# Kernel tuning notes

Measured on AMD Instinct MI355X. Metric: run time of the kernel, lower is better.

## Reference

```python
import jax, jax.numpy as jnp
from jax import lax
import numpy as np

DIM, RESO, HEADS, SPLIT, B = 128, 112, 4, 7, 2
HID = 4 * DIM  # mlp_ratio=4


def _ln(x, g, b):
    m = x.mean(-1, keepdims=True)
    v = ((x - m) ** 2).mean(-1, keepdims=True)
    return (x - m) * lax.rsqrt(v + 1e-5) * g + b


def _lepe_attn(q, k, v, cw, cb, H, W, H_sp, W_sp, nh):
    # q,k,v: [B, H*W, C] (C = branch dim); cw: depthwise conv weight [C,1,3,3]
    Bq, L, C = q.shape
    hd = C // nh
    scale = hd ** -0.5
    nHw, nWw = H // H_sp, W // W_sp

    def to_win(t):  # [B,H,W,C] -> [B*nHw*nWw, nh, H_sp*W_sp, hd]
        t = t.reshape(Bq, nHw, H_sp, nWw, W_sp, C).transpose(0, 1, 3, 2, 4, 5)
        return t.reshape(-1, H_sp * W_sp, nh, hd).transpose(0, 2, 1, 3)

    qw = to_win(q.reshape(Bq, H, W, C)) * scale
    kw = to_win(k.reshape(Bq, H, W, C))

    # v path: window partition in NCHW, depthwise conv LePE per window
    vimg = v.transpose(0, 2, 1).reshape(Bq, C, H, W)
    vimg = vimg.reshape(Bq, C, nHw, H_sp, nWw, W_sp).transpose(0, 2, 4, 1, 3, 5)
    vimg = vimg.reshape(-1, C, H_sp, W_sp)  # [B', C, H_sp, W_sp]
    lepe = lax.conv_general_dilated(vimg, cw, (1, 1), 'SAME', feature_group_count=C,
                                    dimension_numbers=('NCHW', 'OIHW', 'NCHW'))
    lepe = lepe + cb[None, :, None, None]
    vw = vimg.reshape(-1, nh, hd, H_sp * W_sp).transpose(0, 1, 3, 2)
    lepe = lepe.reshape(-1, nh, hd, H_sp * W_sp).transpose(0, 1, 3, 2)

    attn = jax.nn.softmax(jnp.einsum('whnd,whmd->whnm', qw, kw), axis=-1)
    o = jnp.einsum('whnm,whmd->whnd', attn, vw) + lepe  # [B', nh, S, hd]

    # windows2img
    o = o.transpose(0, 2, 1, 3).reshape(-1, H_sp * W_sp, C)
    o = o.reshape(Bq, nHw, nWw, H_sp, W_sp, C).transpose(0, 1, 3, 2, 4, 5)
    return o.reshape(Bq, H * W, C)


def setup_inputs() -> dict:
    key = jax.random.key(0)
    ks = jax.random.split(key, 16)
    s = 0.02
    Cb = DIM // 2
    return {
        'x': jax.random.normal(ks[0], (B, RESO * RESO, DIM), jnp.float32),
        'g1': jnp.ones((DIM,), jnp.float32),
        'b1': jnp.zeros((DIM,), jnp.float32),
        'w_qkv': s * jax.random.normal(ks[1], (3 * DIM, DIM), jnp.float32),
        'conv_w0': s * jax.random.normal(ks[2], (Cb, 1, 3, 3), jnp.float32),
        'conv_b0': jnp.zeros((Cb,), jnp.float32),
        'conv_w1': s * jax.random.normal(ks[3], (Cb, 1, 3, 3), jnp.float32),
        'conv_b1': jnp.zeros((Cb,), jnp.float32),
        'w_proj': s * jax.random.normal(ks[4], (DIM, DIM), jnp.float32),
        'b_proj': jnp.zeros((DIM,), jnp.float32),
        'g2': jnp.ones((DIM,), jnp.float32),
        'b2': jnp.zeros((DIM,), jnp.float32),
        'w_fc1': s * jax.random.normal(ks[5], (HID, DIM), jnp.float32),
        'b_fc1': jnp.zeros((HID,), jnp.float32),
        'w_fc2': s * jax.random.normal(ks[6], (DIM, HID), jnp.float32),
        'b_fc2': jnp.zeros((DIM,), jnp.float32),
    }


def reference(x, g1, b1, w_qkv, conv_w0, conv_b0, conv_w1, conv_b1,
              w_proj, b_proj, g2, b2, w_fc1, b_fc1, w_fc2, b_fc2):
    Bq, L, C = x.shape
    Cb = C // 2
    nh_b = HEADS // 2
    img = _ln(x, g1, b1)
    qkv = (img @ w_qkv.T).reshape(Bq, L, 3, C)  # qkv_bias=False
    q, k, v = qkv[:, :, 0], qkv[:, :, 1], qkv[:, :, 2]
    # branch 0: horizontal stripes (H_sp=RESO, W_sp=SPLIT) on first half of channels
    x1 = _lepe_attn(q[..., :Cb], k[..., :Cb], v[..., :Cb], conv_w0, conv_b0,
                    RESO, RESO, RESO, SPLIT, nh_b)
    # branch 1: vertical stripes (H_sp=SPLIT, W_sp=RESO) on second half
    x2 = _lepe_attn(q[..., Cb:], k[..., Cb:], v[..., Cb:], conv_w1, conv_b1,
                    RESO, RESO, SPLIT, RESO, nh_b)
    att = jnp.concatenate([x1, x2], axis=2)
    att = att @ w_proj.T + b_proj
    x = x + att  # drop_path = identity (prob 0)
    y = _ln(x, g2, b2)
    h = jax.nn.gelu(y @ w_fc1.T + b_fc1, approximate=False)
    x = x + (h @ w_fc2.T + b_fc2)
    return x
```

## Files before the change

### kernel.cpp

```cpp
#include <hip/hip_runtime.h>
#include <cstdint>

#define LTOK 12544
#define BATCH 2
#define CDIM 128
#define C3 384
#define RES 112
#define NROWS (BATCH * LTOK)
#define SCALE 0.17677669529663687f

typedef __attribute__((ext_vector_type(8))) short bf16x8;
typedef __attribute__((ext_vector_type(4))) float f32x4;

__device__ inline ushort f2b(float f) {
    union { float f; unsigned u; } v; v.f = f;
    unsigned r = (v.u + 0x7FFFu + ((v.u >> 16) & 1u)) >> 16;
    return (ushort)r;
}
__device__ inline float b2f(ushort u) {
    union { float f; unsigned u; } v; v.u = ((unsigned)u) << 16; return v.f;
}
__device__ inline float gelu_f(float a) {
    return 0.5f * a * (1.0f + erff(a * 0.70710678118654752f));
}

__device__ inline void nij(int n, int branch, int& i, int& j) {
    if (branch == 0) { i = n / 7; j = n - i * 7; }
    else             { i = n / 112; j = n - i * 112; }
}

__global__ __launch_bounds__(256) void k_cvt(const float* __restrict__ w0, const float* __restrict__ w1,
        const float* __restrict__ w2, const float* __restrict__ w3,
        ushort* __restrict__ o0, ushort* __restrict__ o1,
        ushort* __restrict__ o2, ushort* __restrict__ o3)
{
    int idx = blockIdx.x * 256 + threadIdx.x;
    const float* src; ushort* dst; int vi;
    if      (idx < 12288) { src = w0; dst = o0; vi = idx; }
    else if (idx < 16384) { src = w1; dst = o1; vi = idx - 12288; }
    else if (idx < 32768) { src = w2; dst = o2; vi = idx - 16384; }
    else                  { src = w3; dst = o3; vi = idx - 32768; }
    float4 v = ((const float4*)src)[vi];
    ushort4 r; r.x = f2b(v.x); r.y = f2b(v.y); r.z = f2b(v.z); r.w = f2b(v.w);
    ((ushort4*)dst)[vi] = r;
}

__global__ __launch_bounds__(256) void k_ln_qkv(const float* __restrict__ x,
        const float* __restrict__ g1, const float* __restrict__ b1,
        const ushort* __restrict__ wqkv_bf, ushort* __restrict__ qkv)
{
    __shared__ ushort ys[32][136];
    const int tid = threadIdx.x;
    const long long row0 = (long long)blockIdx.x * 32;

    {
        const int r = tid >> 3, l8 = tid & 7;
        const float* xr = x + (row0 + r) * CDIM + l8 * 16;
        float4 a[4];
        #pragma unroll
        for (int i = 0; i < 4; ++i) a[i] = ((const float4*)xr)[i];
        float s = 0.f, s2 = 0.f;
        #pragma unroll
        for (int i = 0; i < 4; ++i) {
            s  += a[i].x + a[i].y + a[i].z + a[i].w;
            s2 += a[i].x*a[i].x + a[i].y*a[i].y + a[i].z*a[i].z + a[i].w*a[i].w;
        }
        #pragma unroll
        for (int m = 4; m >= 1; m >>= 1) { s += __shfl_xor(s, m, 8); s2 += __shfl_xor(s2, m, 8); }
        const float mean = s * (1.f / 128.f);
        const float var = s2 * (1.f / 128.f) - mean * mean;
        const float rs = rsqrtf(var + 1e-5f);
        ushort4 w[4];
        #pragma unroll
        for (int i = 0; i < 4; ++i) {
            float4 gg = *(const float4*)(g1 + l8 * 16 + i * 4);
            float4 bb = *(const float4*)(b1 + l8 * 16 + i * 4);
            w[i].x = f2b((a[i].x - mean) * rs * gg.x + bb.x);
            w[i].y = f2b((a[i].y - mean) * rs * gg.y + bb.y);
            w[i].z = f2b((a[i].z - mean) * rs * gg.z + bb.z);
            w[i].w = f2b((a[i].w - mean) * rs * gg.w + bb.w);
        }
        #pragma unroll
        for (int i = 0; i < 4; ++i) *(ushort4*)&ys[r][l8 * 16 + i * 4] = w[i];
    }
    __syncthreads();

    const int wv = tid >> 6, lane = tid & 63;
    const int c16 = lane & 15, g = lane >> 4;

    bf16x8 yb[2][4];
    #pragma unroll
    for (int mt = 0; mt < 2; ++mt)
        #pragma unroll
        for (int kc = 0; kc < 4; ++kc)
            yb[mt][kc] = *(const bf16x8*)&ys[mt * 16 + c16][kc * 32 + g * 8];

    #pragma unroll
    for (int t = 0; t < 6; ++t) {
        const int n0 = wv * 96 + t * 16;
        bf16x8 aw[4];
        #pragma unroll
        for (int kc = 0; kc < 4; ++kc)
            aw[kc] = *(const bf16x8*)&wqkv_bf[(n0 + c16) * CDIM + kc * 32 + g * 8];
        #pragma unroll
        for (int mt = 0; mt < 2; ++mt) {
            f32x4 acc = {0.f, 0.f, 0.f, 0.f};
            #pragma unroll
            for (int kc = 0; kc < 4; ++kc)
                acc = __builtin_amdgcn_mfma_f32_16x16x32_bf16(aw[kc], yb[mt][kc], acc, 0, 0, 0);
            ushort4 sv;
            sv.x = f2b(acc[0]); sv.y = f2b(acc[1]); sv.z = f2b(acc[2]); sv.w = f2b(acc[3]);
            *(ushort4*)&qkv[(row0 + mt * 16 + c16) * C3 + n0 + g * 4] = sv;
        }
    }
}

__global__ __launch_bounds__(256) void k_attn_mfma(const ushort* __restrict__ qkv,
        const float* __restrict__ cw0, const float* __restrict__ cb0,
        const float* __restrict__ cw1, const float* __restrict__ cb1,
        ushort* __restrict__ att)
{
    __shared__ __align__(16) ushort ks[112 * 40];
    __shared__ __align__(16) ushort vt[32 * 136];
    __shared__ __align__(16) ushort pl[4][16 * 40];
    __shared__ __align__(16) float  ol[4][16 * 36];

    const int tid = threadIdx.x;
    const int wv = tid >> 6, lane = tid & 63;
    const int g = lane >> 4, c16 = lane & 15;

    const int wh = blockIdx.x;
    const int branch = wh >> 6;
    const int idx = wh & 63;
    const int win = idx >> 1, head = idx & 1;
    const int b = win >> 4, w = win & 15;
    const int rowBase = branch ? w * 7 : 0;
    const int colBase = branch ? 0 : w * 7;
    const float* cw = branch ? cw1 : cw0;
    const float* cb = branch ? cb1 : cb0;
    const int cbase = branch * 64 + head * 32;
    const long long qkvB = (long long)b * LTOK * C3;

    {
        const int row = tid >> 3, cwd = tid & 7;
        *(unsigned*)&vt[row * 136 + 112 + cwd * 2] = 0u;
    }

    const int t0 = blockIdx.y * 7 + 2 * wv;
    const int nt = (2 * wv + 1 < 7) ? 2 : 1;

    bf16x8 qf[2];
    #pragma unroll
    for (int t = 0; t < 2; ++t) if (t < nt) {
        int n = (t0 + t) * 16 + c16;
        int i, j; nij(n, branch, i, j);
        const ushort* qp = qkv + qkvB + (long long)((rowBase + i) * RES + colBase + j) * C3 + cbase + g * 8;
        bf16x8 qq = *(const bf16x8*)qp;
        #pragma unroll
        for (int e = 0; e < 8; ++e) qq[e] = (short)f2b(b2f((ushort)qq[e]) * SCALE);
        qf[t] = qq;
    }

    f32x4 O00 = {0.f,0.f,0.f,0.f}, O01 = {0.f,0.f,0.f,0.f};
    f32x4 O10 = {0.f,0.f,0.f,0.f}, O11 = {0.f,0.f,0.f,0.f};
    float lsum0[4] = {0.f,0.f,0.f,0.f};
    float lsum1[4] = {0.f,0.f,0.f,0.f};

    for (int cc = 0; cc < 7; ++cc) {
        __syncthreads();
        for (int u = tid; u < 448; u += 256) {
            const int key = u >> 2, d8 = (u & 3) * 8;
            const int n = cc * 112 + key;
            int i, j; nij(n, branch, i, j);
            const ushort* base = qkv + qkvB + (long long)((rowBase + i) * RES + colBase + j) * C3 + cbase + d8;
            bf16x8 kk = *(const bf16x8*)(base + 128);
            bf16x8 vv = *(const bf16x8*)(base + 256);
            *(bf16x8*)&ks[key * 40 + d8] = kk;
            #pragma unroll
            for (int e = 0; e < 8; ++e) vt[(d8 + e) * 136 + key] = (ushort)vv[e];
        }
        __syncthreads();

        #pragma unroll
        for (int p = 0; p < 4; ++p) {
            bf16x8 kf0 = *(const bf16x8*)&ks[(p * 32 + c16) * 40 + g * 8];
            bf16x8 kf1;
            if (p < 3) kf1 = *(const bf16x8*)&ks[(p * 32 + 16 + c16) * 40 + g * 8];
            bf16x8 vf0 = *(const bf16x8*)&vt[c16 * 136 + p * 32 + g * 8];
            bf16x8 vf1 = *(const bf16x8*)&vt[(16 + c16) * 136 + p * 32 + g * 8];
            ushort* pb = &pl[wv][0];

            #pragma unroll
            for (int t = 0; t < 2; ++t) if (t < nt) {
                const bf16x8 qq = t ? qf[1] : qf[0];
                f32x4 z = {0.f,0.f,0.f,0.f};
                f32x4 S0 = __builtin_amdgcn_mfma_f32_16x16x32_bf16(qq, kf0, z, 0, 0, 0);
                f32x4 S1 = z;
                if (p < 3) S1 = __builtin_amdgcn_mfma_f32_16x16x32_bf16(qq, kf1, z, 0, 0, 0);
                ushort pw0[4], pw1[4];
                #pragma unroll
                for (int r = 0; r < 4; ++r) {
                    float e0 = __expf(S0[r]);
                    if (t) lsum1[r] += e0; else lsum0[r] += e0;
                    pw0[r] = f2b(e0);
                    if (p < 3) {
                        float e1 = __expf(S1[r]);
                        if (t) lsum1[r] += e1; else lsum0[r] += e1;
                        pw1[r] = f2b(e1);
                    } else pw1[r] = 0;
                }
                #pragma unroll
                for (int r = 0; r < 4; ++r) {
                    pb[(g * 4 + r) * 40 + c16]      = pw0[r];
                    pb[(g * 4 + r) * 40 + 16 + c16] = pw1[r];
                }
                bf16x8 pf = *(const bf16x8*)&pb[c16 * 40 + g * 8];
                if (t) {
                    O10 = __builtin_amdgcn_mfma_f32_16x16x32_bf16(pf, vf0, O10, 0, 0, 0);
                    O11 = __builtin_amdgcn_mfma_f32_16x16x32_bf16(pf, vf1, O11, 0, 0, 0);
                } else {
                    O00 = __builtin_amdgcn_mfma_f32_16x16x32_bf16(pf, vf0, O00, 0, 0, 0);
                    O01 = __builtin_amdgcn_mfma_f32_16x16x32_bf16(pf, vf1, O01, 0, 0, 0);
                }
            }
        }
    }

    const int H_sp = branch ? 7 : RES;
    const int W_sp = branch ? RES : 7;
    #pragma unroll
    for (int t = 0; t < 2; ++t) if (t < nt) {
        float* ob = &ol[wv][0];
        #pragma unroll
        for (int r = 0; r < 4; ++r) {
            float s = t ? lsum1[r] : lsum0[r];
            s += __shfl_xor(s, 1); s += __shfl_xor(s, 2);
            s += __shfl_xor(s, 4); s += __shfl_xor(s, 8);
            const float inv = 1.f / s;
            const f32x4 Oa = t ? O10 : O00;
            const f32x4 Ob = t ? O11 : O01;
            ob[(g * 4 + r) * 36 + c16]      = Oa[r] * inv;
            ob[(g * 4 + r) * 36 + 16 + c16] = Ob[r] * inv;
        }
        const int r2 = lane >> 2, db = (lane & 3) * 8;
        const int n0 = (t0 + t) * 16 + r2;
        int i0, j0; nij(n0, branch, i0, j0);
        float acc[8];
        #pragma unroll
        for (int e = 0; e < 8; ++e) acc[e] = ob[r2 * 36 + db + e] + cb[head * 32 + db + e];
        #pragma unroll
        for (int dij = 0; dij < 9; ++dij) {
            const int di = dij / 3 - 1, dj = dij % 3 - 1;
            const int ii = i0 + di, jj = j0 + dj;
            if (ii >= 0 && ii < H_sp && jj >= 0 && jj < W_sp) {
                const ushort* vp = qkv + qkvB + (long long)((rowBase + ii) * RES + colBase + jj) * C3 + 256 + cbase + db;
                bf16x8 vv = *(const bf16x8*)vp;
                #pragma unroll
                for (int e = 0; e < 8; ++e)
                    acc[e] += cw[(head * 32 + db + e) * 9 + dij] * b2f((ushort)vv[e]);
            }
        }
        const long long Lq = (long long)(rowBase + i0) * RES + colBase + j0;
        ushort* op = att + ((long long)b * LTOK + Lq) * CDIM + cbase + db;
        bf16x8 ov;
        #pragma unroll
        for (int e = 0; e < 8; ++e) ov[e] = (short)f2b(acc[e]);
        *(bf16x8*)op = ov;
    }
}

__global__ __launch_bounds__(256) void k_proj(const ushort* __restrict__ att,
        const ushort* __restrict__ wproj_bf, const float* __restrict__ bproj,
        const float* __restrict__ x, float* __restrict__ xmid)
{
    const int tid = threadIdx.x;
    const int wv = tid >> 6, lane = tid & 63;
    const int c16 = lane & 15, g = lane >> 4;
    const long long row0 = (long long)blockIdx.x * 64;

    bf16x8 ab[4][4];
    #pragma unroll
    for (int mt = 0; mt < 4; ++mt)
        #pragma unroll
        for (int kc = 0; kc < 4; ++kc)
            ab[mt][kc] = *(const bf16x8*)&att[(row0 + mt * 16 + c16) * CDIM + kc * 32 + g * 8];

    #pragma unroll
    for (int tt = 0; tt < 2; ++tt) {
        const int n2 = wv * 32 + tt * 16;
        bf16x8 aw[4];
        #pragma unroll
        for (int kc = 0; kc < 4; ++kc)
            aw[kc] = *(const bf16x8*)&wproj_bf[(n2 + c16) * CDIM + kc * 32 + g * 8];
        f32x4 acc[4] = {{0.f,0.f,0.f,0.f},{0.f,0.f,0.f,0.f},{0.f,0.f,0.f,0.f},{0.f,0.f,0.f,0.f}};
        #pragma unroll
        for (int kc = 0; kc < 4; ++kc)
            #pragma unroll
            for (int mt = 0; mt < 4; ++mt)
                acc[mt] = __builtin_amdgcn_mfma_f32_16x16x32_bf16(aw[kc], ab[mt][kc], acc[mt], 0, 0, 0);
        const int col = n2 + g * 4;
        float4 bb = *(const float4*)&bproj[col];
        #pragma unroll
        for (int mt = 0; mt < 4; ++mt) {
            const long long row = row0 + mt * 16 + c16;
            float4 xv = *(const float4*)&x[row * CDIM + col];
            float4 o;
            o.x = acc[mt][0] + xv.x + bb.x;
            o.y = acc[mt][1] + xv.y + bb.y;
            o.z = acc[mt][2] + xv.z + bb.z;
            o.w = acc[mt][3] + xv.w + bb.w;
            *(float4*)&xmid[row * CDIM + col] = o;
        }
    }
}

__global__ __launch_bounds__(256) void k_mlp(const float* __restrict__ xmid,
        const float* __restrict__ g2, const float* __restrict__ b2,
        const ushort* __restrict__ w1bf, const float* __restrict__ bfc1,
        const ushort* __restrict__ w2bf, const float* __restrict__ bfc2,
        float* __restrict__ out)
{
    __shared__ ushort ys[64][136];
    __shared__ ushort hs[64][264];
    const int tid = threadIdx.x;
    const long long row0 = (long long)blockIdx.x * 64;

    {
        const int r = tid >> 2, t4 = tid & 3;
        const float* xr = xmid + (row0 + r) * CDIM + t4 * 32;
        float4 a[8];
        #pragma unroll
        for (int i = 0; i < 8; ++i) a[i] = ((const float4*)xr)[i];
        float s = 0.f, s2 = 0.f;
        #pragma unroll
        for (int i = 0; i < 8; ++i) {
            s  += a[i].x + a[i].y + a[i].z + a[i].w;
            s2 += a[i].x*a[i].x + a[i].y*a[i].y + a[i].z*a[i].z + a[i].w*a[i].w;
        }
        s += __shfl_xor(s, 1, 4); s2 += __shfl_xor(s2, 1, 4);
        s += __shfl_xor(s, 2, 4); s2 += __shfl_xor(s2, 2, 4);
        const float mean = s * (1.f / 128.f);
        const float var = s2 * (1.f / 128.f) - mean * mean;
        const float rs = rsqrtf(var + 1e-5f);
        #pragma unroll
        for (int i = 0; i < 8; i += 2) {
            ushort4 w0, w1;
            float4 ga = *(const float4*)(g2 + t4 * 32 + i * 4);
            float4 ba = *(const float4*)(b2 + t4 * 32 + i * 4);
            float4 gb = *(const float4*)(g2 + t4 * 32 + i * 4 + 4);
            float4 bb = *(const float4*)(b2 + t4 * 32 + i * 4 + 4);
            w0.x = f2b((a[i].x - mean) * rs * ga.x + ba.x);
            w0.y = f2b((a[i].y - mean) * rs * ga.y + ba.y);
            w0.z = f2b((a[i].z - mean) * rs * ga.z + ba.z);
            w0.w = f2b((a[i].w - mean) * rs * ga.w + ba.w);
            w1.x = f2b((a[i+1].x - mean) * rs * gb.x + bb.x);
            w1.y = f2b((a[i+1].y - mean) * rs * gb.y + bb.y);
            w1.z = f2b((a[i+1].z - mean) * rs * gb.z + bb.z);
            w1.w = f2b((a[i+1].w - mean) * rs * gb.w + bb.w);
            *(ushort4*)&ys[r][t4 * 32 + i * 4]     = w0;
            *(ushort4*)&ys[r][t4 * 32 + i * 4 + 4] = w1;
        }
    }
    __syncthreads();

    const int wv = tid >> 6, lane = tid & 63;
    const int c16 = lane & 15, g = lane >> 4;

    bf16x8 yb[4][4];
    #pragma unroll
    for (int mt = 0; mt < 4; ++mt)
        #pragma unroll
        for (int kc = 0; kc < 4; ++kc)
            yb[mt][kc] = *(const bf16x8*)&ys[mt * 16 + c16][kc * 32 + g * 8];

    f32x4 acc2[2][4];
    #pragma unroll
    for (int tt = 0; tt < 2; ++tt)
        #pragma unroll
        for (int mt = 0; mt < 4; ++mt)
            acc2[tt][mt] = (f32x4){0.f, 0.f, 0.f, 0.f};

    #pragma unroll
    for (int half = 0; half < 2; ++half) {
        #pragma unroll
        for (int t = 0; t < 4; ++t) {
            const int n0g = half * 256 + wv * 64 + t * 16;
            bf16x8 aw[4];
            #pragma unroll
            for (int kc = 0; kc < 4; ++kc)
                aw[kc] = *(const bf16x8*)&w1bf[(n0g + c16) * CDIM + kc * 32 + g * 8];
            float4 b1v = *(const float4*)&bfc1[n0g + g * 4];
            #pragma unroll
            for (int mt = 0; mt < 4; ++mt) {
                f32x4 a = {0.f, 0.f, 0.f, 0.f};
                #pragma unroll
                for (int kc = 0; kc < 4; ++kc)
                    a = __builtin_amdgcn_mfma_f32_16x16x32_bf16(aw[kc], yb[mt][kc], a, 0, 0, 0);
                ushort4 sv;
                sv.x = f2b(gelu_f(a[0] + b1v.x));
                sv.y = f2b(gelu_f(a[1] + b1v.y));
                sv.z = f2b(gelu_f(a[2] + b1v.z));
                sv.w = f2b(gelu_f(a[3] + b1v.w));
                *(ushort4*)&hs[mt * 16 + c16][wv * 64 + t * 16 + g * 4] = sv;
            }
        }
        __syncthreads();

        #pragma unroll
        for (int kc = 0; kc < 8; ++kc) {
            bf16x8 hb[4];
            #pragma unroll
            for (int mt = 0; mt < 4; ++mt)
                hb[mt] = *(const bf16x8*)&hs[mt * 16 + c16][kc * 32 + g * 8];
            #pragma unroll
            for (int tt = 0; tt < 2; ++tt) {
                bf16x8 aw2 = *(const bf16x8*)&w2bf[(wv * 32 + tt * 16 + c16) * 512 + half * 256 + kc * 32 + g * 8];
                #pragma unroll
                for (int mt = 0; mt < 4; ++mt)
                    acc2[tt][mt] = __builtin_amdgcn_mfma_f32_16x16x32_bf16(aw2, hb[mt], acc2[tt][mt], 0, 0, 0);
            }
        }
        if (half == 0) __syncthreads();
    }

    #pragma unroll
    for (int tt = 0; tt < 2; ++tt) {
        const int col = wv * 32 + tt * 16 + g * 4;
        float4 bb = *(const float4*)&bfc2[col];
        #pragma unroll
        for (int mt = 0; mt < 4; ++mt) {
            const long long row = row0 + mt * 16 + c16;
            float4 res = *(const float4*)&xmid[row * CDIM + col];
            float4 o;
            o.x = acc2[tt][mt][0] + res.x + bb.x;
            o.y = acc2[tt][mt][1] + res.y + bb.y;
            o.z = acc2[tt][mt][2] + res.z + bb.z;
            o.w = acc2[tt][mt][3] + res.w + bb.w;
            *(float4*)&out[row * CDIM + col] = o;
        }
    }
}

extern "C" void kernel_launch(void* const* d_in, const int* in_sizes, int n_in,
                              void* d_out, int out_size, void* d_ws, size_t ws_size,
                              hipStream_t stream) {
    const float* x     = (const float*)d_in[0];
    const float* g1    = (const float*)d_in[1];
    const float* b1    = (const float*)d_in[2];
    const float* wqkv  = (const float*)d_in[3];
    const float* cw0   = (const float*)d_in[4];
    const float* cb0   = (const float*)d_in[5];
    const float* cw1   = (const float*)d_in[6];
    const float* cb1   = (const float*)d_in[7];
    const float* wproj = (const float*)d_in[8];
    const float* bproj = (const float*)d_in[9];
    const float* g2    = (const float*)d_in[10];
    const float* b2    = (const float*)d_in[11];
    const float* wfc1  = (const float*)d_in[12];
    const float* bfc1  = (const float*)d_in[13];
    const float* wfc2  = (const float*)d_in[14];
    const float* bfc2  = (const float*)d_in[15];

    char* wsb = (char*)d_ws;
    ushort* qkv_bf   = (ushort*)wsb;
    ushort* att_bf   = (ushort*)(wsb + 19267584);
    float*  xmid     = (float*) (wsb + 19267584 + 6422528);
    char*   wbase    = wsb + 38535168;
    ushort* wqkv_bf  = (ushort*)(wbase);
    ushort* wproj_bf = (ushort*)(wbase + 98304);
    ushort* wfc1_bf  = (ushort*)(wbase + 98304 + 32768);
    ushort* wfc2_bf  = (ushort*)(wbase + 98304 + 32768 + 131072);

    float* out = (float*)d_out;

    k_cvt<<<192, 256, 0, stream>>>(wqkv, wproj, wfc1, wfc2, wqkv_bf, wproj_bf, wfc1_bf, wfc2_bf);
    k_ln_qkv<<<NROWS / 32, 256, 0, stream>>>(x, g1, b1, wqkv_bf, qkv_bf);
    k_attn_mfma<<<dim3(128, 7), 256, 0, stream>>>(qkv_bf, cw0, cb0, cw1, cb1, att_bf);
    k_proj<<<NROWS / 64, 256, 0, stream>>>(att_bf, wproj_bf, bproj, x, xmid);
    k_mlp<<<NROWS / 64, 256, 0, stream>>>(xmid, g2, b2, wfc1_bf, bfc1, wfc2_bf, bfc2, out);
}
```

Measured before the change: 126.2 us.

## Fuse output projection into MLP kernel, keep residual in registers and LDS

Merges the projection GEMM with the LN2+MLP kernel so the fp32 intermediate (xmid) is no longer written to and re-read from global memory. The projection result is staged in a shared-memory union (reused later for the hidden activations) for the LayerNorm and kept in registers as the residual. The row tile shrinks from 64 to 32 to fit the LDS budget and launch twice as many blocks. The cost is reloading weights from cache twice as often per row.

```diff
diff --git a/kernel.cpp b/kernel.cpp
--- a/kernel.cpp
+++ b/kernel.cpp
@@ -269,115 +269,103 @@
     }
 }
 
-__global__ __launch_bounds__(256) void k_proj(const ushort* __restrict__ att,
+__global__ __launch_bounds__(256) void k_pmlp(const ushort* __restrict__ att,
         const ushort* __restrict__ wproj_bf, const float* __restrict__ bproj,
-        const float* __restrict__ x, float* __restrict__ xmid)
-{
-    const int tid = threadIdx.x;
-    const int wv = tid >> 6, lane = tid & 63;
-    const int c16 = lane & 15, g = lane >> 4;
-    const long long row0 = (long long)blockIdx.x * 64;
-
-    bf16x8 ab[4][4];
-    #pragma unroll
-    for (int mt = 0; mt < 4; ++mt)
-        #pragma unroll
-        for (int kc = 0; kc < 4; ++kc)
-            ab[mt][kc] = *(const bf16x8*)&att[(row0 + mt * 16 + c16) * CDIM + kc * 32 + g * 8];
-
-    #pragma unroll
-    for (int tt = 0; tt < 2; ++tt) {
-        const int n2 = wv * 32 + tt * 16;
-        bf16x8 aw[4];
-        #pragma unroll
-        for (int kc = 0; kc < 4; ++kc)
-            aw[kc] = *(const bf16x8*)&wproj_bf[(n2 + c16) * CDIM + kc * 32 + g * 8];
-        f32x4 acc[4] = {{0.f,0.f,0.f,0.f},{0.f,0.f,0.f,0.f},{0.f,0.f,0.f,0.f},{0.f,0.f,0.f,0.f}};
-        #pragma unroll
-        for (int kc = 0; kc < 4; ++kc)
-            #pragma unroll
-            for (int mt = 0; mt < 4; ++mt)
-                acc[mt] = __builtin_amdgcn_mfma_f32_16x16x32_bf16(aw[kc], ab[mt][kc], acc[mt], 0, 0, 0);
-        const int col = n2 + g * 4;
-        float4 bb = *(const float4*)&bproj[col];
-        #pragma unroll
-        for (int mt = 0; mt < 4; ++mt) {
-            const long long row = row0 + mt * 16 + c16;
-            float4 xv = *(const float4*)&x[row * CDIM + col];
-            float4 o;
-            o.x = acc[mt][0] + xv.x + bb.x;
-            o.y = acc[mt][1] + xv.y + bb.y;
-            o.z = acc[mt][2] + xv.z + bb.z;
-            o.w = acc[mt][3] + xv.w + bb.w;
-            *(float4*)&xmid[row * CDIM + col] = o;
-        }
-    }
-}
-
-__global__ __launch_bounds__(256) void k_mlp(const float* __restrict__ xmid,
+        const float* __restrict__ x,
         const float* __restrict__ g2, const float* __restrict__ b2,
         const ushort* __restrict__ w1bf, const float* __restrict__ bfc1,
         const ushort* __restrict__ w2bf, const float* __restrict__ bfc2,
         float* __restrict__ out)
 {
-    __shared__ ushort ys[64][136];
-    __shared__ ushort hs[64][264];
+    __shared__ union {
+        float  xs[32][132];
+        ushort hs[32][264];
+    } u;
+    __shared__ ushort ys[32][136];
     const int tid = threadIdx.x;
-    const long long row0 = (long long)blockIdx.x * 64;
-
+    const int wv = tid >> 6, lane = tid & 63;
+    const int c16 = lane & 15, g = lane >> 4;
+    const long long row0 = (long long)blockIdx.x * 32;
+
+    f32x4 resid[2][2];
     {
-        const int r = tid >> 2, t4 = tid & 3;
-        const float* xr = xmid + (row0 + r) * CDIM + t4 * 32;
-        float4 a[8];
-        #pragma unroll
-        for (int i = 0; i < 8; ++i) a[i] = ((const float4*)xr)[i];
+        bf16x8 ab[2][4];
+        #pragma unroll
+        for (int mt = 0; mt < 2; ++mt)
+            #pragma unroll
+            for (int kc = 0; kc < 4; ++kc)
+                ab[mt][kc] = *(const bf16x8*)&att[(row0 + mt * 16 + c16) * CDIM + kc * 32 + g * 8];
+
+        #pragma unroll
+        for (int tt = 0; tt < 2; ++tt) {
+            const int n2 = wv * 32 + tt * 16;
+            bf16x8 aw[4];
+            #pragma unroll
+            for (int kc = 0; kc < 4; ++kc)
+                aw[kc] = *(const bf16x8*)&wproj_bf[(n2 + c16) * CDIM + kc * 32 + g * 8];
+            const int col = n2 + g * 4;
+            float4 bb = *(const float4*)&bproj[col];
+            #pragma unroll
+            for (int mt = 0; mt < 2; ++mt) {
+                f32x4 a = {0.f, 0.f, 0.f, 0.f};
+                #pragma unroll
+                for (int kc = 0; kc < 4; ++kc)
+                    a = __builtin_amdgcn_mfma_f32_16x16x32_bf16(aw[kc], ab[mt][kc], a, 0, 0, 0);
+                float4 xv = *(const float4*)&x[(row0 + mt * 16 + c16) * CDIM + col];
+                f32x4 r;
+                r[0] = a[0] + xv.x + bb.x;
+                r[1] = a[1] + xv.y + bb.y;
+                r[2] = a[2] + xv.z + bb.z;
+                r[3] = a[3] + xv.w + bb.w;
+                resid[tt][mt] = r;
+                *(float4*)&u.xs[mt * 16 + c16][col] = make_float4(r[0], r[1], r[2], r[3]);
+            }
+        }
+    }
+    __syncthreads();
+
+    {
+        const int r = tid >> 3, l8 = tid & 7;
+        float4 a[4];
+        #pragma unroll
+        for (int i = 0; i < 4; ++i) a[i] = *(const float4*)&u.xs[r][l8 * 16 + i * 4];
         float s = 0.f, s2 = 0.f;
         #pragma unroll
-        for (int i = 0; i < 8; ++i) {
+        for (int i = 0; i < 4; ++i) {
             s  += a[i].x + a[i].y + a[i].z + a[i].w;
             s2 += a[i].x*a[i].x + a[i].y*a[i].y + a[i].z*a[i].z + a[i].w*a[i].w;
         }
-        s += __shfl_xor(s, 1, 4); s2 += __shfl_xor(s2, 1, 4);
-        s += __shfl_xor(s, 2, 4); s2 += __shfl_xor(s2, 2, 4);
+        #pragma unroll
+        for (int m = 4; m >= 1; m >>= 1) { s += __shfl_xor(s, m, 8); s2 += __shfl_xor(s2, m, 8); }
         const float mean = s * (1.f / 128.f);
         const float var = s2 * (1.f / 128.f) - mean * mean;
         const float rs = rsqrtf(var + 1e-5f);
         #pragma unroll
-        for (int i = 0; i < 8; i += 2) {
-            ushort4 w0, w1;
-            float4 ga = *(const float4*)(g2 + t4 * 32 + i * 4);
-            float4 ba = *(const float4*)(b2 + t4 * 32 + i * 4);
-            float4 gb = *(const float4*)(g2 + t4 * 32 + i * 4 + 4);
-            float4 bb = *(const float4*)(b2 + t4 * 32 + i * 4 + 4);
-            w0.x = f2b((a[i].x - mean) * rs * ga.x + ba.x);
-            w0.y = f2b((a[i].y - mean) * rs * ga.y + ba.y);
-            w0.z = f2b((a[i].z - mean) * rs * ga.z + ba.z);
-            w0.w = f2b((a[i].w - mean) * rs * ga.w + ba.w);
-            w1.x = f2b((a[i+1].x - mean) * rs * gb.x + bb.x);
-            w1.y = f2b((a[i+1].y - mean) * rs * gb.y + bb.y);
-            w1.z = f2b((a[i+1].z - mean) * rs * gb.z + bb.z);
-            w1.w = f2b((a[i+1].w - mean) * rs * gb.w + bb.w);
-            *(ushort4*)&ys[r][t4 * 32 + i * 4]     = w0;
-            *(ushort4*)&ys[r][t4 * 32 + i * 4 + 4] = w1;
+        for (int i = 0; i < 4; ++i) {
+            float4 gg = *(const float4*)(g2 + l8 * 16 + i * 4);
+            float4 bb = *(const float4*)(b2 + l8 * 16 + i * 4);
+            ushort4 w;
+            w.x = f2b((a[i].x - mean) * rs * gg.x + bb.x);
+            w.y = f2b((a[i].y - mean) * rs * gg.y + bb.y);
+            w.z = f2b((a[i].z - mean) * rs * gg.z + bb.z);
+            w.w = f2b((a[i].w - mean) * rs * gg.w + bb.w);
+            *(ushort4*)&ys[r][l8 * 16 + i * 4] = w;
         }
     }
     __syncthreads();
 
-    const int wv = tid >> 6, lane = tid & 63;
-    const int c16 = lane & 15, g = lane >> 4;
-
-    bf16x8 yb[4][4];
-    #pragma unroll
-    for (int mt = 0; mt < 4; ++mt)
+    bf16x8 yb[2][4];
+    #pragma unroll
+    for (int mt = 0; mt < 2; ++mt)
         #pragma unroll
         for (int kc = 0; kc < 4; ++kc)
             yb[mt][kc] = *(const bf16x8*)&ys[mt * 16 + c16][kc * 32 + g * 8];
 
-    f32x4 acc2[2][4];
+    f32x4 acc2[2][2];
     #pragma unroll
     for (int tt = 0; tt < 2; ++tt)
         #pragma unroll
-        for (int mt = 0; mt < 4; ++mt)
+        for (int mt = 0; mt < 2; ++mt)
             acc2[tt][mt] = (f32x4){0.f, 0.f, 0.f, 0.f};
 
     #pragma unroll
@@ -391,7 +379,7 @@
                 aw[kc] = *(const bf16x8*)&w1bf[(n0g + c16) * CDIM + kc * 32 + g * 8];
             float4 b1v = *(const float4*)&bfc1[n0g + g * 4];
             #pragma unroll
-            for (int mt = 0; mt < 4; ++mt) {
+            for (int mt = 0; mt < 2; ++mt) {
                 f32x4 a = {0.f, 0.f, 0.f, 0.f};
                 #pragma unroll
                 for (int kc = 0; kc < 4; ++kc)
@@ -401,22 +389,22 @@
                 sv.y = f2b(gelu_f(a[1] + b1v.y));
                 sv.z = f2b(gelu_f(a[2] + b1v.z));
                 sv.w = f2b(gelu_f(a[3] + b1v.w));
-                *(ushort4*)&hs[mt * 16 + c16][wv * 64 + t * 16 + g * 4] = sv;
+                *(ushort4*)&u.hs[mt * 16 + c16][wv * 64 + t * 16 + g * 4] = sv;
             }
         }
         __syncthreads();
 
         #pragma unroll
         for (int kc = 0; kc < 8; ++kc) {
-            bf16x8 hb[4];
-            #pragma unroll
-            for (int mt = 0; mt < 4; ++mt)
-                hb[mt] = *(const bf16x8*)&hs[mt * 16 + c16][kc * 32 + g * 8];
+            bf16x8 hb[2];
+            #pragma unroll
+            for (int mt = 0; mt < 2; ++mt)
+                hb[mt] = *(const bf16x8*)&u.hs[mt * 16 + c16][kc * 32 + g * 8];
             #pragma unroll
             for (int tt = 0; tt < 2; ++tt) {
                 bf16x8 aw2 = *(const bf16x8*)&w2bf[(wv * 32 + tt * 16 + c16) * 512 + half * 256 + kc * 32 + g * 8];
                 #pragma unroll
-                for (int mt = 0; mt < 4; ++mt)
+                for (int mt = 0; mt < 2; ++mt)
                     acc2[tt][mt] = __builtin_amdgcn_mfma_f32_16x16x32_bf16(aw2, hb[mt], acc2[tt][mt], 0, 0, 0);
             }
         }
@@ -428,14 +416,13 @@
         const int col = wv * 32 + tt * 16 + g * 4;
         float4 bb = *(const float4*)&bfc2[col];
         #pragma unroll
-        for (int mt = 0; mt < 4; ++mt) {
+        for (int mt = 0; mt < 2; ++mt) {
             const long long row = row0 + mt * 16 + c16;
-            float4 res = *(const float4*)&xmid[row * CDIM + col];
             float4 o;
-            o.x = acc2[tt][mt][0] + res.x + bb.x;
-            o.y = acc2[tt][mt][1] + res.y + bb.y;
-            o.z = acc2[tt][mt][2] + res.z + bb.z;
-            o.w = acc2[tt][mt][3] + res.w + bb.w;
+            o.x = acc2[tt][mt][0] + resid[tt][mt][0] + bb.x;
+            o.y = acc2[tt][mt][1] + resid[tt][mt][1] + bb.y;
+            o.z = acc2[tt][mt][2] + resid[tt][mt][2] + bb.z;
+            o.w = acc2[tt][mt][3] + resid[tt][mt][3] + bb.w;
             *(float4*)&out[row * CDIM + col] = o;
         }
     }
@@ -464,8 +451,7 @@
     char* wsb = (char*)d_ws;
     ushort* qkv_bf   = (ushort*)wsb;
     ushort* att_bf   = (ushort*)(wsb + 19267584);
-    float*  xmid     = (float*) (wsb + 19267584 + 6422528);
-    char*   wbase    = wsb + 38535168;
+    char*   wbase    = wsb + 19267584 + 6422528;
     ushort* wqkv_bf  = (ushort*)(wbase);
     ushort* wproj_bf = (ushort*)(wbase + 98304);
     ushort* wfc1_bf  = (ushort*)(wbase + 98304 + 32768);
@@ -476,6 +462,6 @@
     k_cvt<<<192, 256, 0, stream>>>(wqkv, wproj, wfc1, wfc2, wqkv_bf, wproj_bf, wfc1_bf, wfc2_bf);
     k_ln_qkv<<<NROWS / 32, 256, 0, stream>>>(x, g1, b1, wqkv_bf, qkv_bf);
     k_attn_mfma<<<dim3(128, 7), 256, 0, stream>>>(qkv_bf, cw0, cb0, cw1, cb1, att_bf);
-    k_proj<<<NROWS / 64, 256, 0, stream>>>(att_bf, wproj_bf, bproj, x, xmid);
-    k_mlp<<<NROWS / 64, 256, 0, stream>>>(xmid, g2, b2, wfc1_bf, bfc1, wfc2_bf, bfc2, out);
-}
+    k_pmlp<<<NROWS / 32, 256, 0, stream>>>(att_bf, wproj_bf, bproj, x, g2, b2,
+                                           wfc1_bf, bfc1, wfc2_bf, bfc2, out);
+}
```

Measured after the change: 115.6 us. -8.4%, faster.
